# Kernel optimization log

Hardware: AMD Instinct MI355X
Metric: run time of the kernel (lower is better)

Reference implementation:

```python
import jax, jax.numpy as jnp
import numpy as np

N = 768        # particles
C0 = 16        # input L0 channels
TDIM = 8       # time embedding channels
NB = 32        # sinusoidal rbf bases
H = 32         # hidden channels per L
NITERS = 2     # diffusion iterations (hk.scan length)
RCUT = 6.0     # rbf length scale
EPS = 1e-8

_lc = np.zeros((3, 3, 3), dtype=np.float32)
_lc[0, 1, 2] = _lc[1, 2, 0] = _lc[2, 0, 1] = 1.0
_lc[0, 2, 1] = _lc[2, 1, 0] = _lc[1, 0, 2] = -1.0
LEVI_CIVITA = jnp.asarray(_lc)


def setup_inputs() -> dict:
    key = jax.random.key(0)
    ks = jax.random.split(key, 20)
    s = 0.05
    inp = {
        "positions":   jax.random.normal(ks[0], (N, 3)),
        "features_L0": jax.random.normal(ks[1], (N, C0, 1)),
        "tw1": s * jax.random.normal(ks[2], (1, 32)),
        "tb1": jnp.zeros((32,)),
        "tw2": s * jax.random.normal(ks[3], (32, TDIM)),
        "tb2": jnp.zeros((TDIM,)),
        "R0_00": s * jax.random.normal(ks[4], (NB, C0 + TDIM)),
        "R0_01": s * jax.random.normal(ks[5], (NB, C0 + TDIM)),
        "W0_L0": s * jax.random.normal(ks[6], (C0 + TDIM, H)),
        "b0_L0": jnp.zeros((H,)),
        "W0_L1": s * jax.random.normal(ks[7], (C0 + TDIM, H)),
        "R1_00":  s * jax.random.normal(ks[8], (NB, H)),
        "R1_11d": s * jax.random.normal(ks[9], (NB, H)),
        "R1_01":  s * jax.random.normal(ks[10], (NB, H)),
        "R1_10":  s * jax.random.normal(ks[11], (NB, H)),
        "R1_11c": s * jax.random.normal(ks[12], (NB, H)),
        "W1_L0": s * jax.random.normal(ks[13], (2 * H, 1)),
        "b1_L0": jnp.zeros((1,)),
        "W1_L1": s * jax.random.normal(ks[14], (3 * H, 2)),
        "hutch_seed": 0,
    }
    return inp


def reference(positions, features_L0, tw1, tb1, tw2, tb2,
              R0_00, R0_01, W0_L0, b0_L0, W0_L1,
              R1_00, R1_11d, R1_01, R1_10, R1_11c,
              W1_L0, b1_L0, W1_L1, hutch_seed):
    freqs = jnp.arange(1, NB + 1, dtype=jnp.float32) * (np.pi / RCUT)
    key0 = jax.random.key(hutch_seed)

    def step(carry, it):
        pos, key = carry
        # pairwise displacements / norms / unit vectors, diagonal masked to 0
        r = pos[:, None, :] - pos[None, :, :]                 # (N,N,3)
        n2 = jnp.sum(r * r, axis=-1)                          # (N,N)
        norms = jnp.sqrt(n2 + EPS)
        valid = n2 > 1e-10
        safe = jnp.where(valid, norms, 1.0)
        unit = r / safe[..., None]                            # (N,N,3)
        # sinusoidal radial basis, masked on diagonal (mask_value = 0)
        rbf = jnp.where(valid[..., None],
                        jnp.sin(norms[..., None] * freqs) / safe[..., None],
                        0.0)                                   # (N,N,NB)
        # time convolution MLP, appended as extra L0 channels
        t = (it.astype(jnp.float32) + 1.0) / NITERS
        th = jax.nn.swish(jnp.array([t]) @ tw1 + tb1)
        tvec = th @ tw2 + tb2                                  # (TDIM,)
        aug = jnp.concatenate(
            [features_L0, jnp.broadcast_to(tvec[None, :, None], (N, TDIM, 1))],
            axis=1)                                            # (N,C0+TDIM,1)
        f0 = aug[..., 0]                                       # (N,C0+TDIM)

        # ---- layer 0: conv (L0 input only) + per-L MLP (nonlinear) ----
        Rw = jnp.einsum('ijb,bc->ijc', rbf, R0_00)
        o0 = jnp.einsum('ijc,jc->ic', Rw, f0)[..., None]       # (N,C,1)
        Rw = jnp.einsum('ijb,bc->ijc', rbf, R0_01)
        o1 = jnp.einsum('ijc,jc,ijm->icm', Rw, f0, unit)       # (N,C,3)
        x0 = jax.nn.swish(jnp.einsum('nco,ch->nho', o0, W0_L0)
                          + b0_L0[None, :, None])              # (N,H,1)
        v1 = jnp.einsum('ncm,ch->nhm', o1, W0_L1)
        gate = jax.nn.sigmoid(jnp.sqrt(jnp.sum(v1 * v1, -1) + EPS))
        x1 = v1 * gate[..., None]                              # (N,H,3)

        # ---- layer 1: full L={0,1} TFN conv + linear output MLPs ----
        f0b = x0[..., 0]
        Rw = jnp.einsum('ijb,bc->ijc', rbf, R1_00)
        o0a = jnp.einsum('ijc,jc->ic', Rw, f0b)                # 0x0->0
        Rw = jnp.einsum('ijb,bc->ijc', rbf, R1_11d)
        o0b = jnp.einsum('ijc,jcm,ijm->ic', Rw, x1, unit)      # 1x1->0 (dot)
        o0 = jnp.concatenate([o0a, o0b], axis=-1)[..., None]   # (N,2H,1)
        Rw = jnp.einsum('ijb,bc->ijc', rbf, R1_01)
        o1a = jnp.einsum('ijc,jc,ijm->icm', Rw, f0b, unit)     # 0x1->1
        Rw = jnp.einsum('ijb,bc->ijc', rbf, R1_10)
        o1b = jnp.einsum('ijc,jcm->icm', Rw, x1)               # 1x0->1
        Rw = jnp.einsum('ijb,bc->ijc', rbf, R1_11c)
        o1c = jnp.einsum('ijc,jca,ijb,abm->icm', Rw, x1, unit, LEVI_CIVITA)  # 1x1->1 (cross)
        o1 = jnp.concatenate([o1a, o1b, o1c], axis=1)          # (N,3H,3)
        y0 = jnp.einsum('nco,ch->nho', o0, W1_L0) + b1_L0[None, :, None]  # (N,1,1)
        y1 = jnp.einsum('ncm,ch->nhm', o1, W1_L1)              # (N,2,3)

        # output head: log-sigma from L0 channel 0, translation from L1 channel 1
        sigmas = jnp.repeat(jnp.exp(y0[:, 0, :]), repeats=3, axis=-1)  # (N,3)
        translations = y1[:, 1, :]
        mu = pos + translations
        key, hkey = jax.random.split(key)
        noise = jax.random.normal(hkey, (N, 3))
        out_y = mu + noise * sigmas
        logp = jax.scipy.stats.norm.logpdf(out_y, loc=mu, scale=sigmas).sum()
        return (out_y, key), (out_y, logp)

    (out_pos, _), (ys, logps) = jax.lax.scan(
        step, (positions, key0), jnp.arange(NITERS))
    out_ys = jnp.concatenate([positions[None], ys], axis=0)   # (NITERS+1,N,3)
    return out_pos, jnp.sum(logps), out_ys
```

## Files before the change

### kernel.cpp

```cpp
#include <hip/hip_runtime.h>
#include <hip/hip_bf16.h>
#include <stdint.h>

#define WS_MODE  0
#define WS_PX    16
#define WS_PY    784
#define WS_PZ    1552
#define WS_TVEC  2320
#define WS_HKEY  2336
#define WS_FEATT 2352
#define WS_W0L0  14640
#define WS_B0L0  15408
#define WS_W0L1  15440
#define WS_W1L0  16208
#define WS_B1L0  16272
#define WS_W1L1  16288
#define WS_R00T  16480
#define WS_R01T  17248
#define WS_R1F   18016
#define WS_GT    23136
#define WS_PA    293472
#define WS_PB    293472
#define WS_LG    735840

#define OUT_LOGP 2304
#define OUT_YS   2305

__device__ __forceinline__ float ld_in(const void* p, int idx, int bf) {
  if (bf) return __bfloat162float(((const __hip_bfloat16*)p)[idx]);
  return ((const float*)p)[idx];
}
__device__ __forceinline__ void store_out(void* out, int idx, float v, int bf) {
  if (bf) ((__hip_bfloat16*)out)[idx] = __float2bfloat16(v);
  else ((float*)out)[idx] = v;
}

__device__ __forceinline__ void tf2x32(uint32_t k0, uint32_t k1, uint32_t x0, uint32_t x1,
                                       uint32_t& o0, uint32_t& o1) {
  uint32_t ks[3] = {k0, k1, k0 ^ k1 ^ 0x1BD11BDAu};
  x0 += ks[0]; x1 += ks[1];
  const int R0[4] = {13, 15, 26, 6};
  const int R1[4] = {17, 29, 16, 24};
#pragma unroll
  for (int i = 0; i < 5; ++i) {
    const int* r = (i & 1) ? R1 : R0;
#pragma unroll
    for (int q = 0; q < 4; ++q) {
      x0 += x1;
      x1 = (x1 << r[q]) | (x1 >> (32 - r[q]));
      x1 ^= x0;
    }
    x0 += ks[(i + 1) % 3];
    x1 += ks[(i + 2) % 3] + (uint32_t)(i + 1);
  }
  o0 = x0; o1 = x1;
}

__device__ __forceinline__ float erfinv_f(float x) {
  float w = -log1pf(-x * x);
  float p;
  if (w < 5.0f) {
    w -= 2.5f;
    p = 2.81022636e-08f;
    p = fmaf(p, w, 3.43273939e-07f);
    p = fmaf(p, w, -3.5233877e-06f);
    p = fmaf(p, w, -4.39150654e-06f);
    p = fmaf(p, w, 0.00021858087f);
    p = fmaf(p, w, -0.00125372503f);
    p = fmaf(p, w, -0.00417768164f);
    p = fmaf(p, w, 0.246640727f);
    p = fmaf(p, w, 1.50140941f);
  } else {
    w = sqrtf(w) - 3.0f;
    p = -0.000200214257f;
    p = fmaf(p, w, 0.000100950558f);
    p = fmaf(p, w, 0.00134934322f);
    p = fmaf(p, w, -0.00367342844f);
    p = fmaf(p, w, 0.00573950773f);
    p = fmaf(p, w, -0.0076224613f);
    p = fmaf(p, w, 0.00943887047f);
    p = fmaf(p, w, 1.00167406f);
    p = fmaf(p, w, 2.83297682f);
  }
  return p * x;
}

__device__ int probe_bf(const void* pos, int tid) {
  __shared__ int s_ok;
  if (tid == 0) s_ok = 1;
  __syncthreads();
  const unsigned short* ph = (const unsigned short*)pos;
  int ok = 1;
  for (int e = tid; e < 2304; e += 256) {
    unsigned short v = ph[e];
    if ((v & 0x7fffu) != 0u) {
      int ex = (v >> 7) & 0xff;
      if (ex < 40 || ex > 140) ok = 0;
    }
  }
  if (!ok) atomicAnd(&s_ok, 0);
  __syncthreads();
  return s_ok;
}

__global__ __launch_bounds__(256) void k_init(
    const void* pos, const void* feats, const void* tw1, const void* tb1,
    const void* tw2, const void* tb2, const void* R000, const void* R001,
    const void* W0L0, const void* b0L0, const void* W0L1,
    const void* R100, const void* R111d, const void* R101,
    const void* R110, const void* R111c,
    const void* W1L0, const void* b1L0, const void* W1L1,
    const int* seedp, float* ws, void* out) {
  int tid = threadIdx.x, b = blockIdx.x;
  int bf = probe_bf(pos, tid);
  switch (b) {
    case 0: {
      if (tid == 0) ws[WS_MODE] = (float)bf;
      if (tid < 16) {
        int it = tid >> 3, d = tid & 7;
        float t = (float)(it + 1) * 0.5f;
        float a = ld_in(tb2, d, bf);
        for (int h = 0; h < 32; ++h) {
          float pre = fmaf(t, ld_in(tw1, h, bf), ld_in(tb1, h, bf));
          float th = pre / (1.0f + expf(-pre));
          a = fmaf(th, ld_in(tw2, h * 8 + d, bf), a);
        }
        ws[WS_TVEC + it * 8 + d] = a;
      }
      if (tid == 32) {
        uint32_t k0 = 0u, k1 = (uint32_t)seedp[0];
        uint32_t* hk = (uint32_t*)(ws + WS_HKEY);
        uint32_t a0, a1, b0, b1, c0, c1;
        tf2x32(k0, k1, 0u, 0u, a0, a1);
        tf2x32(k0, k1, 0u, 1u, b0, b1);
        hk[0] = b0; hk[1] = b1;
        tf2x32(a0, a1, 0u, 1u, c0, c1);
        hk[2] = c0; hk[3] = c1;
      }
      break;
    }
    case 1: {
      for (int n = tid; n < 768; n += 256) {
        ws[WS_PX + n] = ld_in(pos, n * 3 + 0, bf);
        ws[WS_PY + n] = ld_in(pos, n * 3 + 1, bf);
        ws[WS_PZ + n] = ld_in(pos, n * 3 + 2, bf);
      }
      break;
    }
    case 2: case 3: {
      for (int e = (b - 2) * 1152 + tid; e < (b - 1) * 1152; e += 256)
        store_out(out, OUT_YS + e, ld_in(pos, e, bf), bf);
      break;
    }
    case 4: case 5: case 6: case 7:
    case 8: case 9: case 10: case 11: {
      int base = (b - 4) * 1536;
      for (int e = base + tid; e < base + 1536; e += 256) {
        int j = e >> 4, c = e & 15;
        ws[WS_FEATT + c * 768 + j] = ld_in(feats, e, bf);
      }
      break;
    }
    case 12: {
      for (int e = tid; e < 768; e += 256) {
        ws[WS_W0L0 + e] = ld_in(W0L0, e, bf);
        ws[WS_W0L1 + e] = ld_in(W0L1, e, bf);
        ws[WS_R00T + e] = ld_in(R000, e, bf);
        ws[WS_R01T + e] = ld_in(R001, e, bf);
      }
      break;
    }
    case 13: {
      if (tid < 32) ws[WS_B0L0 + tid] = ld_in(b0L0, tid, bf);
      if (tid >= 64 && tid < 128) ws[WS_W1L0 + tid - 64] = ld_in(W1L0, tid - 64, bf);
      if (tid >= 128 && tid < 192) {
        for (int e = tid - 128; e < 192; e += 64) ws[WS_W1L1 + e] = ld_in(W1L1, e, bf);
      }
      if (tid == 33) ws[WS_B1L0] = ld_in(b1L0, 0, bf);
      break;
    }
    case 14: case 15: {
      int base = (b - 14) * 2560;
      const void* tabs[5] = {R100, R111d, R101, R110, R111c};
      for (int e = base + tid; e < base + 2560; e += 256) {
        int tab = e >> 10, off = e & 1023;
        ws[WS_R1F + e] = ld_in(tabs[tab], off, bf);
      }
      break;
    }
  }
}

__global__ __launch_bounds__(256) void k_passA(const float* __restrict__ ws,
                                               float* __restrict__ wso, int it) {
  int i = blockIdx.x, jset = blockIdx.y, CH = blockIdx.z;
  int tid = threadIdx.x, lane = tid & 63, w = tid >> 6;
  int j = jset * 256 + tid;
  float pix = ws[WS_PX + i], piy = ws[WS_PY + i], piz = ws[WS_PZ + i];

  float dx = pix - ws[WS_PX + j];
  float dy = piy - ws[WS_PY + j];
  float dz = piz - ws[WS_PZ + j];
  float n2 = dx * dx + dy * dy + dz * dz;
  float nrm = sqrtf(n2 + 1e-8f);
  float invn = 1.0f / nrm;
  float msk = (n2 > 1e-10f) ? invn : 0.0f;
  float ux = dx * invn, uy = dy * invn, uz = dz * invn;
  float sn, cs;
  sincosf(nrm * 0.52359879f, &sn, &cs);
  float twoc = 2.0f * cs;

  float fv[12];
  const float* __restrict__ rt0 = ws + WS_R00T + CH * 12;
  const float* __restrict__ rt1 = ws + WS_R01T + CH * 12;
  if (CH == 0) {
#pragma unroll
    for (int c = 0; c < 12; ++c) fv[c] = ws[WS_FEATT + c * 768 + j];
  } else {
#pragma unroll
    for (int c = 0; c < 4; ++c) fv[c] = ws[WS_FEATT + (12 + c) * 768 + j];
#pragma unroll
    for (int c = 4; c < 12; ++c) fv[c] = ws[WS_TVEC + it * 8 + (c - 4)];
  }

  float rw0[12], rw1[12];
#pragma unroll
  for (int c = 0; c < 12; ++c) { rw0[c] = 0.0f; rw1[c] = 0.0f; }
  float sk = sn * msk, skm1 = 0.0f;
#pragma unroll
  for (int b = 0; b < 32; ++b) {
#pragma unroll
    for (int c = 0; c < 12; ++c) {
      rw0[c] = fmaf(sk, rt0[b * 24 + c], rw0[c]);
      rw1[c] = fmaf(sk, rt1[b * 24 + c], rw1[c]);
    }
    float s2 = fmaf(twoc, sk, -skm1);
    skm1 = sk; sk = s2;
  }

  float out[48];
#pragma unroll
  for (int c = 0; c < 12; ++c) {
    float f = fv[c];
    out[c] = rw0[c] * f;
    float pp = rw1[c] * f;
    out[12 + 3 * c + 0] = pp * ux;
    out[12 + 3 * c + 1] = pp * uy;
    out[12 + 3 * c + 2] = pp * uz;
  }

#pragma unroll
  for (int k = 0; k < 48; ++k) {
    float v = out[k];
    v += __shfl_xor(v, 1);
    v += __shfl_xor(v, 2);
    out[k] = v;
  }
  __shared__ float P[48][65];
  if ((lane & 3) == 0) {
    int col = w * 16 + (lane >> 2);
#pragma unroll
    for (int k = 0; k < 48; ++k) P[k][col] = out[k];
  }
  __syncthreads();
  if (tid < 48) {
    float s = 0.0f;
#pragma unroll 8
    for (int q = 0; q < 64; ++q) s += P[tid][q];
    wso[WS_PA + ((CH * 3 + jset) * 768 + i) * 48 + tid] = s;
  }
}

__global__ __launch_bounds__(64) void k_passA2(const float* __restrict__ ws,
                                               float* __restrict__ wso) {
  int i = blockIdx.x, lane = threadIdx.x;
  __shared__ float oall[96];
  __shared__ float wf[11][32];
#pragma unroll
  for (int rep = 0; rep < 2; ++rep) {
    int t = rep * 64 + lane;
    if (rep == 0 || lane < 32) {
      int ch, k;
      if (t < 24) { ch = t / 12; k = t % 12; }
      else { int u = t - 24; int c = u / 3, m = u % 3; ch = c / 12; k = 12 + 3 * (c % 12) + m; }
      float s = 0.0f;
#pragma unroll
      for (int js = 0; js < 3; ++js)
        s += ws[WS_PA + ((ch * 3 + js) * 768 + i) * 48 + k];
      oall[t] = s;
    }
  }
  __syncthreads();
  if (lane < 32) {
    int h = lane;
    float x0p = ws[WS_B0L0 + h];
#pragma unroll
    for (int c = 0; c < 24; ++c) x0p = fmaf(oall[c], ws[WS_W0L0 + c * 32 + h], x0p);
    float f0b = x0p / (1.0f + expf(-x0p));
    float v0 = 0.0f, v1 = 0.0f, v2 = 0.0f;
#pragma unroll
    for (int c = 0; c < 24; ++c) {
      float w = ws[WS_W0L1 + c * 32 + h];
      v0 = fmaf(oall[24 + 3 * c + 0], w, v0);
      v1 = fmaf(oall[24 + 3 * c + 1], w, v1);
      v2 = fmaf(oall[24 + 3 * c + 2], w, v2);
    }
    float g = 1.0f / (1.0f + expf(-sqrtf(v0 * v0 + v1 * v1 + v2 * v2 + 1e-8f)));
    float x1m0 = v0 * g, x1m1 = v1 * g, x1m2 = v2 * g;
    float WA = ws[WS_W1L0 + h];
    float WB = ws[WS_W1L0 + 32 + h];
    float Wa = ws[WS_W1L1 + h * 2 + 1];
    float Wb = ws[WS_W1L1 + (32 + h) * 2 + 1];
    float Wc = ws[WS_W1L1 + (64 + h) * 2 + 1];
    wf[0][h] = WA * f0b;
    wf[1][h] = WB * x1m0; wf[2][h] = WB * x1m1; wf[3][h] = WB * x1m2;
    wf[4][h] = Wa * f0b;
    wf[5][h] = Wb * x1m0; wf[6][h] = Wb * x1m1; wf[7][h] = Wb * x1m2;
    wf[8][h] = Wc * x1m0; wf[9][h] = Wc * x1m1; wf[10][h] = Wc * x1m2;
  }
  __syncthreads();
  for (int tt = lane; tt < 352; tt += 64) {
    int comp = tt >> 5, b = tt & 31;
    int tab = (comp == 0) ? 0 : (comp < 4) ? 1 : (comp == 4) ? 2 : (comp < 8) ? 3 : 4;
    const float* rrow = ws + WS_R1F + tab * 1024 + b * 32;
    float gacc = 0.0f;
#pragma unroll
    for (int c = 0; c < 32; ++c) gacc = fmaf(rrow[c], wf[comp][c], gacc);
    wso[WS_GT + i * 352 + tt] = gacc;
  }
}

__global__ __launch_bounds__(64) void k_passB(const float* __restrict__ ws,
                                              float* __restrict__ wso) {
  int i = blockIdx.y * 64 + threadIdx.x;
  int chunk = blockIdx.x;
  float pix = ws[WS_PX + i], piy = ws[WS_PY + i], piz = ws[WS_PZ + i];
  float y0 = 0.0f, t0 = 0.0f, t1 = 0.0f, t2 = 0.0f;
  for (int q = 0; q < 8; ++q) {
    int j = chunk * 8 + q;
    float dx = pix - ws[WS_PX + j];
    float dy = piy - ws[WS_PY + j];
    float dz = piz - ws[WS_PZ + j];
    float n2 = dx * dx + dy * dy + dz * dz;
    float nrm = sqrtf(n2 + 1e-8f);
    float invn = 1.0f / nrm;
    float msk = (n2 > 1e-10f) ? invn : 0.0f;
    float ux = dx * invn, uy = dy * invn, uz = dz * invn;
    float sn, cs;
    sincosf(nrm * 0.52359879f, &sn, &cs);
    float rbf[32];
    float twoc = 2.0f * cs;
    rbf[0] = sn * msk;
    float skm1 = 0.0f, sk = rbf[0];
#pragma unroll
    for (int k = 1; k < 32; ++k) {
      float s2 = fmaf(twoc, sk, -skm1);
      skm1 = sk; sk = s2; rbf[k] = sk;
    }
    const float* g = ws + WS_GT + j * 352;
    float sA = 0.f, vB0 = 0.f, vB1 = 0.f, vB2 = 0.f, sC = 0.f;
    float vD0 = 0.f, vD1 = 0.f, vD2 = 0.f, vE0 = 0.f, vE1 = 0.f, vE2 = 0.f;
#pragma unroll
    for (int b = 0; b < 32; ++b) {
      float r = rbf[b];
      sA  = fmaf(r, g[0 * 32 + b], sA);
      vB0 = fmaf(r, g[1 * 32 + b], vB0);
      vB1 = fmaf(r, g[2 * 32 + b], vB1);
      vB2 = fmaf(r, g[3 * 32 + b], vB2);
      sC  = fmaf(r, g[4 * 32 + b], sC);
      vD0 = fmaf(r, g[5 * 32 + b], vD0);
      vD1 = fmaf(r, g[6 * 32 + b], vD1);
      vD2 = fmaf(r, g[7 * 32 + b], vD2);
      vE0 = fmaf(r, g[8 * 32 + b], vE0);
      vE1 = fmaf(r, g[9 * 32 + b], vE1);
      vE2 = fmaf(r, g[10 * 32 + b], vE2);
    }
    y0 += sA + vB0 * ux + vB1 * uy + vB2 * uz;
    t0 += sC * ux + vD0 + (vE1 * uz - vE2 * uy);
    t1 += sC * uy + vD1 + (vE2 * ux - vE0 * uz);
    t2 += sC * uz + vD2 + (vE0 * uy - vE1 * ux);
  }
  float4* pb = (float4*)(wso + WS_PB);
  pb[i * 96 + chunk] = make_float4(y0, t0, t1, t2);
}

__global__ __launch_bounds__(64) void k_passB2(float* __restrict__ ws, void* out, int it) {
  int i = blockIdx.x * 64 + threadIdx.x;
  int bf = (int)ws[WS_MODE];
  const float4* pb = (const float4*)(ws + WS_PB);
  float ax = 0.f, ay = 0.f, az = 0.f, aw = 0.f;
#pragma unroll 8
  for (int c = 0; c < 96; ++c) {
    float4 v = pb[i * 96 + c];
    ax += v.x; ay += v.y; az += v.z; aw += v.w;
  }
  float y0 = ax + ws[WS_B1L0];
  float sg = expf(y0);
  float s2 = sg * sg;
  float lnrm = 0.5f * logf(6.2831855f * s2);
  const uint32_t* hk = (const uint32_t*)(ws + WS_HKEY);
  uint32_t h0 = hk[it * 2 + 0], h1 = hk[it * 2 + 1];
  float base[3] = {ws[WS_PX + i], ws[WS_PY + i], ws[WS_PZ + i]};
  float tr[3] = {ay, az, aw};
  float logp = 0.0f;
#pragma unroll
  for (int m = 0; m < 3; ++m) {
    float mu = base[m] + tr[m];
    int f = i * 3 + m;
    uint32_t o0, o1;
    tf2x32(h0, h1, 0u, (uint32_t)f, o0, o1);
    uint32_t bits = o0 ^ o1;
    float u1 = __uint_as_float((bits >> 9) | 0x3f800000u) - 1.0f;
    const float lo = -0.99999994f;
    float u = fmaxf(lo, u1 * 2.0f + lo);
    float nz = 1.41421354f * erfinv_f(u);
    float oy = mu + nz * sg;
    float d = oy - mu;
    logp -= lnrm + (d * d) / (2.0f * s2);
    if (m == 0) ws[WS_PX + i] = oy;
    else if (m == 1) ws[WS_PY + i] = oy;
    else ws[WS_PZ + i] = oy;
    store_out(out, OUT_YS + (it + 1) * 2304 + i * 3 + m, oy, bf);
    if (it == 1) store_out(out, i * 3 + m, oy, bf);
  }
  ws[WS_LG + it * 768 + i] = logp;
}

__global__ void k_logp(float* __restrict__ ws, void* out) {
  __shared__ float red[256];
  int t = threadIdx.x;
  float s = 0.0f;
  for (int e = t; e < 1536; e += 256) s += ws[WS_LG + e];
  red[t] = s;
  __syncthreads();
  for (int off = 128; off; off >>= 1) {
    if (t < off) red[t] += red[t + off];
    __syncthreads();
  }
  if (t == 0) store_out(out, OUT_LOGP, red[0], (int)ws[WS_MODE]);
}

extern "C" void kernel_launch(void* const* d_in, const int* in_sizes, int n_in,
                              void* d_out, int out_size, void* d_ws, size_t ws_size,
                              hipStream_t stream) {
  (void)in_sizes; (void)n_in; (void)out_size; (void)ws_size;
  float* ws = (float*)d_ws;
  k_init<<<16, 256, 0, stream>>>(d_in[0], d_in[1], d_in[2], d_in[3], d_in[4], d_in[5],
                                 d_in[6], d_in[7], d_in[8], d_in[9], d_in[10],
                                 d_in[11], d_in[12], d_in[13], d_in[14], d_in[15],
                                 d_in[16], d_in[17], d_in[18], (const int*)d_in[19],
                                 ws, d_out);
  for (int it = 0; it < 2; ++it) {
    k_passA<<<dim3(768, 3, 2), 256, 0, stream>>>(ws, ws, it);
    k_passA2<<<768, 64, 0, stream>>>(ws, ws);
    k_passB<<<dim3(96, 12), 64, 0, stream>>>(ws, ws);
    k_passB2<<<12, 64, 0, stream>>>(ws, d_out, it);
  }
  k_logp<<<1, 256, 0, stream>>>(ws, d_out);
}
```

Before: 189.6 us.

## Fuse reduction kernels into producers via last-block atomic counters

Merges passA2 into passA and passB2 into passB. Per-row atomic counters with thread fences let the last finishing block do the cross-block reduction and the follow-on work. Positions are now double-buffered per iteration, so the in-place update cannot race with other blocks still reading. This cuts four kernel launches and their gaps, in exchange for atomics, fences and an epilogue that runs on only one block per group.

```diff
diff --git a/kernel.cpp b/kernel.cpp
--- a/kernel.cpp
+++ b/kernel.cpp
@@ -3,25 +3,29 @@
 #include <stdint.h>
 
 #define WS_MODE  0
-#define WS_PX    16
-#define WS_PY    784
-#define WS_PZ    1552
-#define WS_TVEC  2320
-#define WS_HKEY  2336
-#define WS_FEATT 2352
-#define WS_W0L0  14640
-#define WS_B0L0  15408
-#define WS_W0L1  15440
-#define WS_W1L0  16208
-#define WS_B1L0  16272
-#define WS_W1L1  16288
-#define WS_R00T  16480
-#define WS_R01T  17248
-#define WS_R1F   18016
-#define WS_GT    23136
-#define WS_PA    293472
-#define WS_PB    293472
-#define WS_LG    735840
+#define WS_TVEC  16
+#define WS_HKEY  32
+#define WS_POS   48
+#define WS_FEATT 6960
+#define WS_W0L0  19248
+#define WS_B0L0  20016
+#define WS_W0L1  20048
+#define WS_W1L0  20816
+#define WS_B1L0  20880
+#define WS_W1L1  20896
+#define WS_R00T  21088
+#define WS_R01T  21856
+#define WS_R1F   22624
+#define WS_CNTA  27744
+#define WS_CNTB  29280
+#define WS_GT    29312
+#define WS_PA    299648
+#define WS_PB    299648
+#define WS_LG    594560
+
+#define POS_X(it) (WS_POS + (it) * 2304)
+#define POS_Y(it) (WS_POS + (it) * 2304 + 768)
+#define POS_Z(it) (WS_POS + (it) * 2304 + 1536)
 
 #define OUT_LOGP 2304
 #define OUT_YS   2305
@@ -141,10 +145,12 @@
     }
     case 1: {
       for (int n = tid; n < 768; n += 256) {
-        ws[WS_PX + n] = ld_in(pos, n * 3 + 0, bf);
-        ws[WS_PY + n] = ld_in(pos, n * 3 + 1, bf);
-        ws[WS_PZ + n] = ld_in(pos, n * 3 + 2, bf);
-      }
+        ws[POS_X(0) + n] = ld_in(pos, n * 3 + 0, bf);
+        ws[POS_Y(0) + n] = ld_in(pos, n * 3 + 1, bf);
+        ws[POS_Z(0) + n] = ld_in(pos, n * 3 + 2, bf);
+      }
+      int* cnt = (int*)ws;
+      for (int e = tid; e < 1560; e += 256) cnt[WS_CNTA + e] = 0;
       break;
     }
     case 2: case 3: {
@@ -196,11 +202,11 @@
   int i = blockIdx.x, jset = blockIdx.y, CH = blockIdx.z;
   int tid = threadIdx.x, lane = tid & 63, w = tid >> 6;
   int j = jset * 256 + tid;
-  float pix = ws[WS_PX + i], piy = ws[WS_PY + i], piz = ws[WS_PZ + i];
-
-  float dx = pix - ws[WS_PX + j];
-  float dy = piy - ws[WS_PY + j];
-  float dz = piz - ws[WS_PZ + j];
+  float pix = ws[POS_X(it) + i], piy = ws[POS_Y(it) + i], piz = ws[POS_Z(it) + i];
+
+  float dx = pix - ws[POS_X(it) + j];
+  float dy = piy - ws[POS_Y(it) + j];
+  float dz = piz - ws[POS_Z(it) + j];
   float n2 = dx * dx + dy * dy + dz * dz;
   float nrm = sqrtf(n2 + 1e-8f);
   float invn = 1.0f / nrm;
@@ -257,6 +263,9 @@
     out[k] = v;
   }
   __shared__ float P[48][65];
+  __shared__ float oall[96];
+  __shared__ float wf[11][32];
+  __shared__ int s_last;
   if ((lane & 3) == 0) {
     int col = w * 16 + (lane >> 2);
 #pragma unroll
@@ -269,30 +278,31 @@
     for (int q = 0; q < 64; ++q) s += P[tid][q];
     wso[WS_PA + ((CH * 3 + jset) * 768 + i) * 48 + tid] = s;
   }
-}
-
-__global__ __launch_bounds__(64) void k_passA2(const float* __restrict__ ws,
-                                               float* __restrict__ wso) {
-  int i = blockIdx.x, lane = threadIdx.x;
-  __shared__ float oall[96];
-  __shared__ float wf[11][32];
-#pragma unroll
-  for (int rep = 0; rep < 2; ++rep) {
-    int t = rep * 64 + lane;
-    if (rep == 0 || lane < 32) {
-      int ch, k;
-      if (t < 24) { ch = t / 12; k = t % 12; }
-      else { int u = t - 24; int c = u / 3, m = u % 3; ch = c / 12; k = 12 + 3 * (c % 12) + m; }
-      float s = 0.0f;
-#pragma unroll
-      for (int js = 0; js < 3; ++js)
-        s += ws[WS_PA + ((ch * 3 + js) * 768 + i) * 48 + k];
-      oall[t] = s;
-    }
-  }
-  __syncthreads();
-  if (lane < 32) {
-    int h = lane;
+  __syncthreads();
+  if (tid == 0) {
+    __threadfence();
+    int* cnt = (int*)wso + (WS_CNTA + it * 768 + i);
+    int prev = atomicAdd(cnt, 1);
+    s_last = (prev == 5) ? 1 : 0;
+  }
+  __syncthreads();
+  if (!s_last) return;
+
+  __threadfence();
+  if (tid < 96) {
+    int t = tid;
+    int ch, k;
+    if (t < 24) { ch = t / 12; k = t % 12; }
+    else { int u = t - 24; int c = u / 3, m = u % 3; ch = c / 12; k = 12 + 3 * (c % 12) + m; }
+    float s = 0.0f;
+#pragma unroll
+    for (int js = 0; js < 3; ++js)
+      s += wso[WS_PA + ((ch * 3 + js) * 768 + i) * 48 + k];
+    oall[t] = s;
+  }
+  __syncthreads();
+  if (tid < 32) {
+    int h = tid;
     float x0p = ws[WS_B0L0 + h];
 #pragma unroll
     for (int c = 0; c < 24; ++c) x0p = fmaf(oall[c], ws[WS_W0L0 + c * 32 + h], x0p);
@@ -300,10 +310,10 @@
     float v0 = 0.0f, v1 = 0.0f, v2 = 0.0f;
 #pragma unroll
     for (int c = 0; c < 24; ++c) {
-      float w = ws[WS_W0L1 + c * 32 + h];
-      v0 = fmaf(oall[24 + 3 * c + 0], w, v0);
-      v1 = fmaf(oall[24 + 3 * c + 1], w, v1);
-      v2 = fmaf(oall[24 + 3 * c + 2], w, v2);
+      float wv = ws[WS_W0L1 + c * 32 + h];
+      v0 = fmaf(oall[24 + 3 * c + 0], wv, v0);
+      v1 = fmaf(oall[24 + 3 * c + 1], wv, v1);
+      v2 = fmaf(oall[24 + 3 * c + 2], wv, v2);
     }
     float g = 1.0f / (1.0f + expf(-sqrtf(v0 * v0 + v1 * v1 + v2 * v2 + 1e-8f)));
     float x1m0 = v0 * g, x1m1 = v1 * g, x1m2 = v2 * g;
@@ -319,7 +329,7 @@
     wf[8][h] = Wc * x1m0; wf[9][h] = Wc * x1m1; wf[10][h] = Wc * x1m2;
   }
   __syncthreads();
-  for (int tt = lane; tt < 352; tt += 64) {
+  for (int tt = tid; tt < 352; tt += 256) {
     int comp = tt >> 5, b = tt & 31;
     int tab = (comp == 0) ? 0 : (comp < 4) ? 1 : (comp == 4) ? 2 : (comp < 8) ? 3 : 4;
     const float* rrow = ws + WS_R1F + tab * 1024 + b * 32;
@@ -331,16 +341,18 @@
 }
 
 __global__ __launch_bounds__(64) void k_passB(const float* __restrict__ ws,
-                                              float* __restrict__ wso) {
-  int i = blockIdx.y * 64 + threadIdx.x;
+                                              float* __restrict__ wso,
+                                              void* out, int it) {
+  int g = blockIdx.y, tid = threadIdx.x;
+  int i = g * 64 + tid;
   int chunk = blockIdx.x;
-  float pix = ws[WS_PX + i], piy = ws[WS_PY + i], piz = ws[WS_PZ + i];
+  float pix = ws[POS_X(it) + i], piy = ws[POS_Y(it) + i], piz = ws[POS_Z(it) + i];
   float y0 = 0.0f, t0 = 0.0f, t1 = 0.0f, t2 = 0.0f;
   for (int q = 0; q < 8; ++q) {
     int j = chunk * 8 + q;
-    float dx = pix - ws[WS_PX + j];
-    float dy = piy - ws[WS_PY + j];
-    float dz = piz - ws[WS_PZ + j];
+    float dx = pix - ws[POS_X(it) + j];
+    float dy = piy - ws[POS_Y(it) + j];
+    float dz = piz - ws[POS_Z(it) + j];
     float n2 = dx * dx + dy * dy + dz * dz;
     float nrm = sqrtf(n2 + 1e-8f);
     float invn = 1.0f / nrm;
@@ -357,23 +369,23 @@
       float s2 = fmaf(twoc, sk, -skm1);
       skm1 = sk; sk = s2; rbf[k] = sk;
     }
-    const float* g = ws + WS_GT + j * 352;
+    const float* gt = ws + WS_GT + j * 352;
     float sA = 0.f, vB0 = 0.f, vB1 = 0.f, vB2 = 0.f, sC = 0.f;
     float vD0 = 0.f, vD1 = 0.f, vD2 = 0.f, vE0 = 0.f, vE1 = 0.f, vE2 = 0.f;
 #pragma unroll
     for (int b = 0; b < 32; ++b) {
       float r = rbf[b];
-      sA  = fmaf(r, g[0 * 32 + b], sA);
-      vB0 = fmaf(r, g[1 * 32 + b], vB0);
-      vB1 = fmaf(r, g[2 * 32 + b], vB1);
-      vB2 = fmaf(r, g[3 * 32 + b], vB2);
-      sC  = fmaf(r, g[4 * 32 + b], sC);
-      vD0 = fmaf(r, g[5 * 32 + b], vD0);
-      vD1 = fmaf(r, g[6 * 32 + b], vD1);
-      vD2 = fmaf(r, g[7 * 32 + b], vD2);
-      vE0 = fmaf(r, g[8 * 32 + b], vE0);
-      vE1 = fmaf(r, g[9 * 32 + b], vE1);
-      vE2 = fmaf(r, g[10 * 32 + b], vE2);
+      sA  = fmaf(r, gt[0 * 32 + b], sA);
+      vB0 = fmaf(r, gt[1 * 32 + b], vB0);
+      vB1 = fmaf(r, gt[2 * 32 + b], vB1);
+      vB2 = fmaf(r, gt[3 * 32 + b], vB2);
+      sC  = fmaf(r, gt[4 * 32 + b], sC);
+      vD0 = fmaf(r, gt[5 * 32 + b], vD0);
+      vD1 = fmaf(r, gt[6 * 32 + b], vD1);
+      vD2 = fmaf(r, gt[7 * 32 + b], vD2);
+      vE0 = fmaf(r, gt[8 * 32 + b], vE0);
+      vE1 = fmaf(r, gt[9 * 32 + b], vE1);
+      vE2 = fmaf(r, gt[10 * 32 + b], vE2);
     }
     y0 += sA + vB0 * ux + vB1 * uy + vB2 * uz;
     t0 += sC * ux + vD0 + (vE1 * uz - vE2 * uy);
@@ -382,25 +394,34 @@
   }
   float4* pb = (float4*)(wso + WS_PB);
   pb[i * 96 + chunk] = make_float4(y0, t0, t1, t2);
-}
-
-__global__ __launch_bounds__(64) void k_passB2(float* __restrict__ ws, void* out, int it) {
-  int i = blockIdx.x * 64 + threadIdx.x;
+
+  __shared__ int s_last;
+  __syncthreads();
+  if (tid == 0) {
+    __threadfence();
+    int* cnt = (int*)wso + (WS_CNTB + it * 12 + g);
+    int prev = atomicAdd(cnt, 1);
+    s_last = (prev == 95) ? 1 : 0;
+  }
+  __syncthreads();
+  if (!s_last) return;
+
+  __threadfence();
   int bf = (int)ws[WS_MODE];
-  const float4* pb = (const float4*)(ws + WS_PB);
+  const float4* pbr = (const float4*)(wso + WS_PB);
   float ax = 0.f, ay = 0.f, az = 0.f, aw = 0.f;
 #pragma unroll 8
   for (int c = 0; c < 96; ++c) {
-    float4 v = pb[i * 96 + c];
+    float4 v = pbr[i * 96 + c];
     ax += v.x; ay += v.y; az += v.z; aw += v.w;
   }
-  float y0 = ax + ws[WS_B1L0];
-  float sg = expf(y0);
-  float s2 = sg * sg;
-  float lnrm = 0.5f * logf(6.2831855f * s2);
+  float y0f = ax + ws[WS_B1L0];
+  float sg = expf(y0f);
+  float s2v = sg * sg;
+  float lnrm = 0.5f * logf(6.2831855f * s2v);
   const uint32_t* hk = (const uint32_t*)(ws + WS_HKEY);
   uint32_t h0 = hk[it * 2 + 0], h1 = hk[it * 2 + 1];
-  float base[3] = {ws[WS_PX + i], ws[WS_PY + i], ws[WS_PZ + i]};
+  float base[3] = {pix, piy, piz};
   float tr[3] = {ay, az, aw};
   float logp = 0.0f;
 #pragma unroll
@@ -416,14 +437,14 @@
     float nz = 1.41421354f * erfinv_f(u);
     float oy = mu + nz * sg;
     float d = oy - mu;
-    logp -= lnrm + (d * d) / (2.0f * s2);
-    if (m == 0) ws[WS_PX + i] = oy;
-    else if (m == 1) ws[WS_PY + i] = oy;
-    else ws[WS_PZ + i] = oy;
+    logp -= lnrm + (d * d) / (2.0f * s2v);
+    if (m == 0) wso[POS_X(it + 1) + i] = oy;
+    else if (m == 1) wso[POS_Y(it + 1) + i] = oy;
+    else wso[POS_Z(it + 1) + i] = oy;
     store_out(out, OUT_YS + (it + 1) * 2304 + i * 3 + m, oy, bf);
     if (it == 1) store_out(out, i * 3 + m, oy, bf);
   }
-  ws[WS_LG + it * 768 + i] = logp;
+  wso[WS_LG + it * 768 + i] = logp;
 }
 
 __global__ void k_logp(float* __restrict__ ws, void* out) {
@@ -452,9 +473,7 @@
                                  ws, d_out);
   for (int it = 0; it < 2; ++it) {
     k_passA<<<dim3(768, 3, 2), 256, 0, stream>>>(ws, ws, it);
-    k_passA2<<<768, 64, 0, stream>>>(ws, ws);
-    k_passB<<<dim3(96, 12), 64, 0, stream>>>(ws, ws);
-    k_passB2<<<12, 64, 0, stream>>>(ws, d_out, it);
+    k_passB<<<dim3(96, 12), 64, 0, stream>>>(ws, ws, d_out, it);
   }
   k_logp<<<1, 256, 0, stream>>>(ws, d_out);
 }
```

Measured after the change: 477.0 us. 2.52x slower.
